# Performance work log

Hardware: AMD Instinct MI355X
Metric: run time of the kernel (lower is better)

Reference implementation:

```python
import jax, jax.numpy as jnp
import numpy as np

NB_CODE = 1024
N, CODE_DIM, T = 32, 512, 2048


def setup_inputs() -> dict:
    key = jax.random.key(0)
    k1, k2 = jax.random.split(key)
    x = jax.random.normal(k1, (N, CODE_DIM, T), dtype=jnp.float32)
    codebook = jax.random.normal(k2, (NB_CODE, CODE_DIM), dtype=jnp.float32)
    return {"x": x, "codebook": codebook}


def reference(x, codebook):
    n, c, t = x.shape
    # preprocess: 'n c t -> (n t) c'
    xf = jnp.transpose(x, (0, 2, 1)).reshape(n * t, c)  # (NT, C)
    dist = (
        jnp.sum(xf * xf, axis=-1, keepdims=True)
        - 2.0 * jnp.matmul(xf, codebook.T)
        + jnp.sum(codebook * codebook, axis=-1)[None, :]
    )
    # gumbel_sample(-distance) with training=False -> plain argmax(-dist) = argmin(dist)
    code_idx = jnp.argmin(dist, axis=-1)  # (NT,) int32
    # dequantize: embedding gather
    x_d = codebook[code_idx]  # (NT, C)
    # compute_perplexity (eval path)
    counts = jax.ops.segment_sum(
        jnp.ones_like(code_idx, dtype=jnp.float32), code_idx, num_segments=NB_CODE
    )
    prob = counts / jnp.sum(counts)
    perplexity = jnp.exp(-jnp.sum(prob * jnp.log(prob + 1e-7)))
    # commit loss against detached quantized codes
    commit_loss = jnp.mean(jnp.square(xf - jax.lax.stop_gradient(x_d)))
    # straight-through estimator
    x_st = xf + jax.lax.stop_gradient(x_d - xf)
    x_out = jnp.transpose(x_st.reshape(n, t, c), (0, 2, 1))  # (N, C, T)
    return x_out, commit_loss, perplexity
```

## Files before the change

### kernel.cpp

```cpp
#include <hip/hip_runtime.h>
#include <stdint.h>

#define N_  32
#define C_  512
#define T_  2048
#define NB  1024
#define NT  (N_ * T_)
#define GB_S 129

typedef _Float16 h8 __attribute__((ext_vector_type(8)));
typedef _Float16 h4 __attribute__((ext_vector_type(4)));
typedef float    f4 __attribute__((ext_vector_type(4)));

#define WS_COMMIT   0
#define WS_COUNTS   64
#define WS_CNORM    4224
#define WS_RMIN     8320
#define WS_CBH      532608
#define WS_CBL      1581184
#define WS_XTH      2629760
#define WS_XTL      69738624
#define WS_NEED     136847488ull

__device__ __forceinline__ void gll16(const void* g, void* l) {
    __builtin_amdgcn_global_load_lds((const __attribute__((address_space(1))) void*)g,
                                     (__attribute__((address_space(3))) void*)l, 16, 0, 0);
}

__global__ void k_initA(unsigned* ws32, unsigned long long* rmin) {
    int g = blockIdx.x * 256 + threadIdx.x;
    if (g < 1040) ws32[g] = 0u;
    rmin[g] = 0xFFFFFFFFFFFFFFFFull;
}

__global__ void k_initS(unsigned* ws32) {
    int g = blockIdx.x * 256 + threadIdx.x;
    if (g < 1040) ws32[g] = 0u;
}

__global__ void k_codenorm(const float* __restrict__ cb, float* __restrict__ cnorm) {
    int j = blockIdx.x * 256 + threadIdx.x;
    const float* r = cb + (size_t)j * C_;
    float s = 0.f;
    for (int i = 0; i < C_; i += 4) {
        float4 v = *(const float4*)&r[i];
        s = fmaf(v.x, v.x, s); s = fmaf(v.y, v.y, s);
        s = fmaf(v.z, v.z, s); s = fmaf(v.w, v.w, s);
    }
    cnorm[j] = s;
}

__global__ void k_cvt_cb(const float* __restrict__ cb,
                         _Float16* __restrict__ cbh, _Float16* __restrict__ cbl) {
    int t = blockIdx.x * 256 + threadIdx.x;
    float4 v = *(const float4*)&cb[(size_t)t * 4];
    h4 hi, lo;
    hi.x = (_Float16)v.x; lo.x = (_Float16)(v.x - (float)hi.x);
    hi.y = (_Float16)v.y; lo.y = (_Float16)(v.y - (float)hi.y);
    hi.z = (_Float16)v.z; lo.z = (_Float16)(v.z - (float)hi.z);
    hi.w = (_Float16)v.w; lo.w = (_Float16)(v.w - (float)hi.w);
    *(h4*)&cbh[(size_t)t * 4] = hi;
    *(h4*)&cbl[(size_t)t * 4] = lo;
}

__global__ __launch_bounds__(256)
void k_xt(const float* __restrict__ x,
          _Float16* __restrict__ xth, _Float16* __restrict__ xtl) {
    __shared__ float Ls[64 * 68];
    const int bx = blockIdx.x;
    const int n = bx >> 8;
    const int cblk = (bx >> 5) & 7, tblk = bx & 31;
    const int c0 = cblk * 64, t0 = tblk * 64;
    const int tid = threadIdx.x;
    #pragma unroll
    for (int ld = 0; ld < 4; ++ld) {
        int idx = tid + ld * 256;
        int cc = idx >> 4, t4 = (idx & 15) << 2;
        float4 v = *(const float4*)&x[((size_t)n * C_ + c0 + cc) * T_ + t0 + t4];
        *(float4*)&Ls[cc * 68 + t4] = v;
    }
    __syncthreads();
    const int tt = tid >> 2, cs = (tid & 3) * 16;
    h8 hi0, hi1, lo0, lo1;
    #pragma unroll
    for (int j = 0; j < 8; ++j) {
        float f = Ls[(cs + j) * 68 + tt];
        _Float16 h = (_Float16)f;
        hi0[j] = h; lo0[j] = (_Float16)(f - (float)h);
    }
    #pragma unroll
    for (int j = 0; j < 8; ++j) {
        float f = Ls[(cs + 8 + j) * 68 + tt];
        _Float16 h = (_Float16)f;
        hi1[j] = h; lo1[j] = (_Float16)(f - (float)h);
    }
    const size_t dst = ((size_t)n * T_ + t0 + tt) * C_ + c0 + cs;
    *(h8*)&xth[dst] = hi0; *(h8*)&xth[dst + 8] = hi1;
    *(h8*)&xtl[dst] = lo0; *(h8*)&xtl[dst + 8] = lo1;
}

__global__ __launch_bounds__(256, 2)
void k_gemm(const _Float16* __restrict__ xth, const _Float16* __restrict__ xtl,
            const _Float16* __restrict__ cbh, const _Float16* __restrict__ cbl,
            const float* __restrict__ cnorm, unsigned long long* __restrict__ rmin) {
    __shared__ _Float16 sm[24576];
    const int tid = threadIdx.x;
    const int l = tid & 63, w = tid >> 6;
    const int q = l >> 4, r = l & 15;
    const int wm0 = (w & 1) * 64, wn0 = (w >> 1) * 128;
    const int bid = blockIdx.x;
    const int lrow = l >> 2;
    const int lcolB = (l & 3) * 16;

    const char* gAh = (const char*)xth + ((size_t)bid * 128 + w * 16 + lrow) * 1024 + lcolB;
    const char* gAl = (const char*)xtl + ((size_t)bid * 128 + w * 16 + lrow) * 1024 + lcolB;

    const int aoff = (wm0 + r) * 32 + q * 8;
    const int boff = (wn0 + r) * 32 + q * 8;

    for (int ch = 0; ch < 4; ++ch) {
        const int j0 = ch * 256;
        const char* gBh = (const char*)cbh + ((size_t)j0 + w * 16 + lrow) * 1024 + lcolB;
        const char* gBl = (const char*)cbl + ((size_t)j0 + w * 16 + lrow) * 1024 + lcolB;

        f4 acc[4][8];
        #pragma unroll
        for (int i = 0; i < 4; ++i)
            #pragma unroll
            for (int j = 0; j < 8; ++j)
                acc[i][j] = (f4){0.f, 0.f, 0.f, 0.f};

        for (int kb = 0; kb < 16; ++kb) {
            const int kof = kb * 64;
            __syncthreads();
            gll16(gAh + kof,         &sm[(size_t)w * 512]);
            gll16(gAh + 65536 + kof, &sm[(size_t)(4 + w) * 512]);
            gll16(gAl + kof,         &sm[4096 + (size_t)w * 512]);
            gll16(gAl + 65536 + kof, &sm[4096 + (size_t)(4 + w) * 512]);
            #pragma unroll
            for (int p = 0; p < 4; ++p) {
                gll16(gBh + (size_t)p * 65536 + kof, &sm[8192  + (size_t)(p * 4 + w) * 512]);
                gll16(gBl + (size_t)p * 65536 + kof, &sm[16384 + (size_t)(p * 4 + w) * 512]);
            }
            __syncthreads();

            h8 ah[4], al[4];
            #pragma unroll
            for (int i = 0; i < 4; ++i) {
                ah[i] = *(const h8*)&sm[aoff + i * 512];
                al[i] = *(const h8*)&sm[4096 + aoff + i * 512];
            }
            #pragma unroll
            for (int j = 0; j < 8; ++j) {
                h8 bh = *(const h8*)&sm[8192  + boff + j * 512];
                h8 bl = *(const h8*)&sm[16384 + boff + j * 512];
                #pragma unroll
                for (int i = 0; i < 4; ++i) {
                    acc[i][j] = __builtin_amdgcn_mfma_f32_16x16x32_f16(ah[i], bh, acc[i][j], 0, 0, 0);
                    acc[i][j] = __builtin_amdgcn_mfma_f32_16x16x32_f16(al[i], bh, acc[i][j], 0, 0, 0);
                    acc[i][j] = __builtin_amdgcn_mfma_f32_16x16x32_f16(ah[i], bl, acc[i][j], 0, 0, 0);
                }
            }
        }

        float cn[8];
        #pragma unroll
        for (int j = 0; j < 8; ++j) cn[j] = cnorm[j0 + wn0 + j * 16 + r];

        #pragma unroll
        for (int i = 0; i < 4; ++i) {
            #pragma unroll
            for (int rg = 0; rg < 4; ++rg) {
                unsigned long long best = 0xFFFFFFFFFFFFFFFFull;
                #pragma unroll
                for (int j = 0; j < 8; ++j) {
                    float s = fmaf(-2.0f, acc[i][j][rg], cn[j]);
                    unsigned u = __float_as_uint(s);
                    u = (u & 0x80000000u) ? ~u : (u | 0x80000000u);
                    unsigned long long key =
                        ((unsigned long long)u << 32) | (unsigned)(j0 + wn0 + j * 16 + r);
                    best = key < best ? key : best;
                }
                #pragma unroll
                for (int off = 1; off < 16; off <<= 1) {
                    unsigned long long o = __shfl_xor(best, off, 64);
                    best = o < best ? o : best;
                }
                if (r == 0)
                    atomicMin(&rmin[(size_t)bid * 128 + wm0 + i * 16 + q * 4 + rg], best);
            }
        }
    }
}

__global__ __launch_bounds__(256)
void k_post(const float* __restrict__ x, const float* __restrict__ cb,
            const unsigned long long* __restrict__ rmin,
            float* __restrict__ out, float* __restrict__ commitAcc,
            int* __restrict__ counts) {
    __shared__ float gbuf[64 * GB_S];
    __shared__ int sidx[128];
    __shared__ float red[4];
    const int bid = blockIdx.x;
    const int tid = threadIdx.x;
    const size_t r0 = (size_t)bid * 128;
    const int n  = (int)(r0 >> 11);
    const int t0 = (int)(r0 & 2047);
    const size_t xbase = (size_t)n * C_ * T_ + t0;

    if (tid < 128) {
        int code = (int)(rmin[r0 + tid] & 0xFFFFFFFFull);
        sidx[tid] = code;
        atomicAdd(&counts[code], 1);
    }
    __syncthreads();

    const int tl   = tid >> 1;
    const int half = tid & 1;
    const int tcol  = tid & 127;
    const int chalf = tid >> 7;
    float commit = 0.f;

    for (int c0 = 0; c0 < C_; c0 += 64) {
        __syncthreads();
        const int code = sidx[tl];
        const float* src = &cb[(size_t)code * C_ + c0 + half * 32];
        #pragma unroll
        for (int qq = 0; qq < 8; ++qq) {
            float4 v = *(const float4*)&src[qq * 4];
            const int cc = half * 32 + qq * 4;
            gbuf[(cc + 0) * GB_S + tl] = v.x;
            gbuf[(cc + 1) * GB_S + tl] = v.y;
            gbuf[(cc + 2) * GB_S + tl] = v.z;
            gbuf[(cc + 3) * GB_S + tl] = v.w;
        }
        __syncthreads();
        #pragma unroll 8
        for (int i = 0; i < 32; ++i) {
            const int cc = i * 2 + chalf;
            const size_t gidx = xbase + (size_t)(c0 + cc) * T_ + tcol;
            float g  = gbuf[cc * GB_S + tcol];
            float xv = x[gidx];
            out[gidx] = g;
            float d = xv - g;
            commit = fmaf(d, d, commit);
        }
    }

    #pragma unroll
    for (int off = 32; off; off >>= 1) commit += __shfl_down(commit, off, 64);
    if ((tid & 63) == 0) red[tid >> 6] = commit;
    __syncthreads();
    if (tid == 0) atomicAdd(commitAcc, red[0] + red[1] + red[2] + red[3]);
}

__global__ void k_final(const int* __restrict__ counts,
                        const float* __restrict__ commitAcc,
                        float* __restrict__ out) {
    __shared__ float red[4];
    int tid = threadIdx.x;
    float s = 0.f;
    for (int j = tid; j < NB; j += 256) {
        float p = (float)counts[j] * (1.0f / (float)NT);
        s += p * logf(p + 1e-7f);
    }
    #pragma unroll
    for (int off = 32; off; off >>= 1) s += __shfl_down(s, off, 64);
    if ((tid & 63) == 0) red[tid >> 6] = s;
    __syncthreads();
    if (tid == 0) {
        float H = red[0] + red[1] + red[2] + red[3];
        out[(size_t)NT * C_]     = commitAcc[0] * (1.0f / ((float)NT * (float)C_));
        out[(size_t)NT * C_ + 1] = expf(-H);
    }
}

#define BM  128
#define BN  128
#define BK  16
#define AS_S 128
#define BS_S 132

__global__ __launch_bounds__(256, 4)
void k_main_fb(const float* __restrict__ x, const float* __restrict__ cb,
               const float* __restrict__ cnorm, float* __restrict__ out,
               float* __restrict__ commitAcc, int* __restrict__ counts) {
    __shared__ float smem[8256];
    __shared__ unsigned long long rmin[BM];
    __shared__ int sidx[BM];
    __shared__ float red[4];

    float* As = smem;
    float* Bs = smem + BK * AS_S;

    const int bid = blockIdx.x;
    const int n   = bid >> 4;
    const int t0  = (bid & 15) << 7;
    const int tid = threadIdx.x;
    const int tx  = tid & 15;
    const int ty  = tid >> 4;

    if (tid < BM) rmin[tid] = 0xFFFFFFFFFFFFFFFFull;

    const size_t xbase = (size_t)n * C_ * T_ + t0;

    for (int ch = 0; ch < NB / BN; ++ch) {
        const int j0 = ch * BN;
        float acc[2][2][4][4];
        #pragma unroll
        for (int a0 = 0; a0 < 2; ++a0)
            #pragma unroll
            for (int a1 = 0; a1 < 2; ++a1)
                #pragma unroll
                for (int a2 = 0; a2 < 4; ++a2)
                    #pragma unroll
                    for (int a3 = 0; a3 < 4; ++a3) acc[a0][a1][a2][a3] = 0.f;

        for (int kb = 0; kb < C_ / BK; ++kb) {
            const int k0 = kb * BK;
            __syncthreads();
            {
                const int kk = tid >> 5;
                const int m4 = (tid & 31) << 2;
                float4 a0v = *(const float4*)&x[xbase + (size_t)(k0 + kk) * T_ + m4];
                float4 a1v = *(const float4*)&x[xbase + (size_t)(k0 + kk + 8) * T_ + m4];
                *(float4*)&As[kk * AS_S + m4] = a0v;
                *(float4*)&As[(kk + 8) * AS_S + m4] = a1v;
                const int j  = tid >> 2;
                const int kq = (tid & 3) << 2;
                float4 b0v = *(const float4*)&cb[(size_t)(j0 + j) * C_ + k0 + kq];
                float4 b1v = *(const float4*)&cb[(size_t)(j0 + j + 64) * C_ + k0 + kq];
                Bs[(kq + 0) * BS_S + j] = b0v.x;
                Bs[(kq + 1) * BS_S + j] = b0v.y;
                Bs[(kq + 2) * BS_S + j] = b0v.z;
                Bs[(kq + 3) * BS_S + j] = b0v.w;
                Bs[(kq + 0) * BS_S + j + 64] = b1v.x;
                Bs[(kq + 1) * BS_S + j + 64] = b1v.y;
                Bs[(kq + 2) * BS_S + j + 64] = b1v.z;
                Bs[(kq + 3) * BS_S + j + 64] = b1v.w;
            }
            __syncthreads();
            #pragma unroll
            for (int kk = 0; kk < BK; ++kk) {
                float4 aL = *(const float4*)&As[kk * AS_S + (ty << 2)];
                float4 aH = *(const float4*)&As[kk * AS_S + 64 + (ty << 2)];
                float4 bL = *(const float4*)&Bs[kk * BS_S + (tx << 2)];
                float4 bH = *(const float4*)&Bs[kk * BS_S + 64 + (tx << 2)];
                float av[2][4] = {{aL.x, aL.y, aL.z, aL.w}, {aH.x, aH.y, aH.z, aH.w}};
                float bv[2][4] = {{bL.x, bL.y, bL.z, bL.w}, {bH.x, bH.y, bH.z, bH.w}};
                #pragma unroll
                for (int ih = 0; ih < 2; ++ih)
                    #pragma unroll
                    for (int i = 0; i < 4; ++i)
                        #pragma unroll
                        for (int jh = 0; jh < 2; ++jh)
                            #pragma unroll
                            for (int j = 0; j < 4; ++j)
                                acc[ih][jh][i][j] = fmaf(av[ih][i], bv[jh][j], acc[ih][jh][i][j]);
            }
        }

        float cnj[2][4];
        #pragma unroll
        for (int jh = 0; jh < 2; ++jh)
            #pragma unroll
            for (int j = 0; j < 4; ++j)
                cnj[jh][j] = cnorm[j0 + jh * 64 + (tx << 2) + j];

        #pragma unroll
        for (int ih = 0; ih < 2; ++ih) {
            #pragma unroll
            for (int i = 0; i < 4; ++i) {
                const int row = ih * 64 + (ty << 2) + i;
                unsigned long long best = 0xFFFFFFFFFFFFFFFFull;
                #pragma unroll
                for (int jh = 0; jh < 2; ++jh) {
                    #pragma unroll
                    for (int j = 0; j < 4; ++j) {
                        const int code = j0 + jh * 64 + (tx << 2) + j;
                        float s = fmaf(-2.0f, acc[ih][jh][i][j], cnj[jh][j]);
                        unsigned u = __float_as_uint(s);
                        u = (u & 0x80000000u) ? ~u : (u | 0x80000000u);
                        unsigned long long key =
                            ((unsigned long long)u << 32) | (unsigned)code;
                        best = key < best ? key : best;
                    }
                }
                #pragma unroll
                for (int off = 8; off; off >>= 1) {
                    unsigned long long o = __shfl_down(best, off, 16);
                    best = o < best ? o : best;
                }
                if (tx == 0) {
                    unsigned long long cur = rmin[row];
                    rmin[row] = best < cur ? best : cur;
                }
            }
        }
    }

    __syncthreads();
    if (tid < BM) {
        int code = (int)(rmin[tid] & 0xFFFFFFFFull);
        sidx[tid] = code;
        atomicAdd(&counts[code], 1);
    }
    __syncthreads();

    float* gbuf = smem;
    const int tl   = tid >> 1;
    const int half = tid & 1;
    const int tcol  = tid & 127;
    const int chalf = tid >> 7;
    float commit = 0.f;

    for (int c0 = 0; c0 < C_; c0 += 64) {
        __syncthreads();
        const int code = sidx[tl];
        const float* src = &cb[(size_t)code * C_ + c0 + half * 32];
        #pragma unroll
        for (int qq = 0; qq < 8; ++qq) {
            float4 v = *(const float4*)&src[qq * 4];
            const int cc = half * 32 + qq * 4;
            gbuf[(cc + 0) * GB_S + tl] = v.x;
            gbuf[(cc + 1) * GB_S + tl] = v.y;
            gbuf[(cc + 2) * GB_S + tl] = v.z;
            gbuf[(cc + 3) * GB_S + tl] = v.w;
        }
        __syncthreads();
        #pragma unroll 8
        for (int i = 0; i < 32; ++i) {
            const int cc = i * 2 + chalf;
            const size_t gidx = xbase + (size_t)(c0 + cc) * T_ + tcol;
            float g  = gbuf[cc * GB_S + tcol];
            float xv = x[gidx];
            out[gidx] = g;
            float d = xv - g;
            commit = fmaf(d, d, commit);
        }
    }

    #pragma unroll
    for (int off = 32; off; off >>= 1) commit += __shfl_down(commit, off, 64);
    if ((tid & 63) == 0) red[tid >> 6] = commit;
    __syncthreads();
    if (tid == 0) atomicAdd(commitAcc, red[0] + red[1] + red[2] + red[3]);
}

extern "C" void kernel_launch(void* const* d_in, const int* in_sizes, int n_in,
                              void* d_out, int out_size, void* d_ws, size_t ws_size,
                              hipStream_t stream) {
    const float* x  = (const float*)d_in[0];
    const float* cb = (const float*)d_in[1];
    float* out = (float*)d_out;

    char* ws = (char*)d_ws;
    float* commitAcc = (float*)(ws + WS_COMMIT);
    int*   counts    = (int*)(ws + WS_COUNTS);
    float* cnorm     = (float*)(ws + WS_CNORM);
    unsigned long long* rmin = (unsigned long long*)(ws + WS_RMIN);
    _Float16* cbh = (_Float16*)(ws + WS_CBH);
    _Float16* cbl = (_Float16*)(ws + WS_CBL);
    _Float16* xth = (_Float16*)(ws + WS_XTH);
    _Float16* xtl = (_Float16*)(ws + WS_XTL);

    if (ws_size >= WS_NEED) {
        k_initA<<<256, 256, 0, stream>>>((unsigned*)ws, rmin);
        k_codenorm<<<4, 256, 0, stream>>>(cb, cnorm);
        k_cvt_cb<<<512, 256, 0, stream>>>(cb, cbh, cbl);
        k_xt<<<8192, 256, 0, stream>>>(x, xth, xtl);
        k_gemm<<<512, 256, 0, stream>>>(xth, xtl, cbh, cbl, cnorm, rmin);
        k_post<<<512, 256, 0, stream>>>(x, cb, rmin, out, commitAcc, counts);
        k_final<<<1, 256, 0, stream>>>(counts, commitAcc, out);
    } else {
        k_initS<<<5, 256, 0, stream>>>((unsigned*)ws);
        k_codenorm<<<4, 256, 0, stream>>>(cb, cnorm);
        k_main_fb<<<512, 256, 0, stream>>>(x, cb, cnorm, out, commitAcc, counts);
        k_final<<<1, 256, 0, stream>>>(counts, commitAcc, out);
    }
}
```

Measured before the change: 544.7 us.

## Retile split-fp16 GEMM with double-buffered LDS and derive commit loss from distances

```diff
diff --git a/kernel.cpp b/kernel.cpp
--- a/kernel.cpp
+++ b/kernel.cpp
@@ -13,6 +13,7 @@
 typedef float    f4 __attribute__((ext_vector_type(4)));
 
 #define WS_COMMIT   0
+#define WS_SUMSQ    8
 #define WS_COUNTS   64
 #define WS_CNORM    4224
 #define WS_RMIN     8320
@@ -65,8 +66,10 @@
 
 __global__ __launch_bounds__(256)
 void k_xt(const float* __restrict__ x,
-          _Float16* __restrict__ xth, _Float16* __restrict__ xtl) {
+          _Float16* __restrict__ xth, _Float16* __restrict__ xtl,
+          float* __restrict__ sumsq) {
     __shared__ float Ls[64 * 68];
+    __shared__ float sred[4];
     const int bx = blockIdx.x;
     const int n = bx >> 8;
     const int cblk = (bx >> 5) & 7, tblk = bx & 31;
@@ -82,119 +85,143 @@
     __syncthreads();
     const int tt = tid >> 2, cs = (tid & 3) * 16;
     h8 hi0, hi1, lo0, lo1;
+    float ss = 0.f;
     #pragma unroll
     for (int j = 0; j < 8; ++j) {
         float f = Ls[(cs + j) * 68 + tt];
+        ss = fmaf(f, f, ss);
         _Float16 h = (_Float16)f;
         hi0[j] = h; lo0[j] = (_Float16)(f - (float)h);
     }
     #pragma unroll
     for (int j = 0; j < 8; ++j) {
         float f = Ls[(cs + 8 + j) * 68 + tt];
+        ss = fmaf(f, f, ss);
         _Float16 h = (_Float16)f;
         hi1[j] = h; lo1[j] = (_Float16)(f - (float)h);
     }
     const size_t dst = ((size_t)n * T_ + t0 + tt) * C_ + c0 + cs;
     *(h8*)&xth[dst] = hi0; *(h8*)&xth[dst + 8] = hi1;
     *(h8*)&xtl[dst] = lo0; *(h8*)&xtl[dst + 8] = lo1;
-}
-
-__global__ __launch_bounds__(256, 2)
+    #pragma unroll
+    for (int off = 32; off; off >>= 1) ss += __shfl_down(ss, off, 64);
+    if ((tid & 63) == 0) sred[tid >> 6] = ss;
+    __syncthreads();
+    if (tid == 0) atomicAdd(sumsq, sred[0] + sred[1] + sred[2] + sred[3]);
+}
+
+__global__ __launch_bounds__(512, 2)
 void k_gemm(const _Float16* __restrict__ xth, const _Float16* __restrict__ xtl,
             const _Float16* __restrict__ cbh, const _Float16* __restrict__ cbl,
             const float* __restrict__ cnorm, unsigned long long* __restrict__ rmin) {
-    __shared__ _Float16 sm[24576];
+    __shared__ __attribute__((aligned(128))) char smc[131072];
     const int tid = threadIdx.x;
     const int l = tid & 63, w = tid >> 6;
     const int q = l >> 4, r = l & 15;
-    const int wm0 = (w & 1) * 64, wn0 = (w >> 1) * 128;
+
     const int bid = blockIdx.x;
-    const int lrow = l >> 2;
-    const int lcolB = (l & 3) * 16;
-
-    const char* gAh = (const char*)xth + ((size_t)bid * 128 + w * 16 + lrow) * 1024 + lcolB;
-    const char* gAl = (const char*)xtl + ((size_t)bid * 128 + w * 16 + lrow) * 1024 + lcolB;
-
-    const int aoff = (wm0 + r) * 32 + q * 8;
-    const int boff = (wn0 + r) * 32 + q * 8;
-
-    for (int ch = 0; ch < 4; ++ch) {
-        const int j0 = ch * 256;
-        const char* gBh = (const char*)cbh + ((size_t)j0 + w * 16 + lrow) * 1024 + lcolB;
-        const char* gBl = (const char*)cbl + ((size_t)j0 + w * 16 + lrow) * 1024 + lcolB;
-
-        f4 acc[4][8];
-        #pragma unroll
-        for (int i = 0; i < 4; ++i)
-            #pragma unroll
-            for (int j = 0; j < 8; ++j)
-                acc[i][j] = (f4){0.f, 0.f, 0.f, 0.f};
-
-        for (int kb = 0; kb < 16; ++kb) {
-            const int kof = kb * 64;
-            __syncthreads();
-            gll16(gAh + kof,         &sm[(size_t)w * 512]);
-            gll16(gAh + 65536 + kof, &sm[(size_t)(4 + w) * 512]);
-            gll16(gAl + kof,         &sm[4096 + (size_t)w * 512]);
-            gll16(gAl + 65536 + kof, &sm[4096 + (size_t)(4 + w) * 512]);
-            #pragma unroll
-            for (int p = 0; p < 4; ++p) {
-                gll16(gBh + (size_t)p * 65536 + kof, &sm[8192  + (size_t)(p * 4 + w) * 512]);
-                gll16(gBl + (size_t)p * 65536 + kof, &sm[16384 + (size_t)(p * 4 + w) * 512]);
+    const int swz = (bid & 7) * 128 + (bid >> 3);
+    const int mb = swz >> 2, nb = swz & 3;
+
+    const char* xthc = (const char*)xth;
+    const char* xtlc = (const char*)xtl;
+    const char* cbhc = (const char*)cbh;
+    const char* cblc = (const char*)cbl;
+
+    const int g16 = l >> 2;
+    const int sslot = ((l & 3) ^ (g16 & 3)) << 4;
+    const int s = w >> 1;
+    const int rhalf = (w & 1) * 128;
+    const char* sbase = (s == 0) ? xthc : (s == 1) ? xtlc : (s == 2) ? cbhc : cblc;
+    const int rowblk = (s < 2) ? (mb * 256) : (nb * 256);
+    const size_t srcOff = ((size_t)(rowblk + rhalf + g16)) * 1024 + sslot;
+    const int ldsOff = s * 16384 + rhalf * 64;
+
+    const int wmi = w & 3, wni = w >> 2;
+    const int slq = (q ^ (r & 3)) << 4;
+    const int aoffb = (wmi * 64 + r) * 64 + slq;
+    const int boffb = 32768 + (wni * 128 + r) * 64 + slq;
+
+    f4 acc[4][8];
+    #pragma unroll
+    for (int i = 0; i < 4; ++i)
+        #pragma unroll
+        for (int j = 0; j < 8; ++j) acc[i][j] = (f4){0.f, 0.f, 0.f, 0.f};
+
+#define STAGE_T(tt, bb) { \
+    const char* sp_ = sbase + srcOff + (tt) * 64; \
+    char* dp_ = smc + (bb) + ldsOff; \
+    _Pragma("unroll") \
+    for (int c_ = 0; c_ < 8; ++c_) gll16(sp_ + c_ * 16384, dp_ + c_ * 1024); }
+
+    STAGE_T(0, 0);
+    asm volatile("s_waitcnt vmcnt(0)" ::: "memory");
+    __builtin_amdgcn_s_barrier();
+
+    int b0 = 0;
+    #pragma unroll 2
+    for (int t = 0; t < 16; ++t) {
+        if (t < 15) STAGE_T(t + 1, b0 ^ 65536);
+        h8 ah[4], al[4];
+        #pragma unroll
+        for (int mf = 0; mf < 4; ++mf) {
+            ah[mf] = *(const h8*)(smc + b0 + aoffb + mf * 1024);
+            al[mf] = *(const h8*)(smc + b0 + 16384 + aoffb + mf * 1024);
+        }
+        __builtin_amdgcn_s_setprio(1);
+        #pragma unroll
+        for (int nf = 0; nf < 8; ++nf) {
+            h8 bhf = *(const h8*)(smc + b0 + boffb + nf * 1024);
+            h8 blf = *(const h8*)(smc + b0 + 16384 + boffb + nf * 1024);
+            #pragma unroll
+            for (int mf = 0; mf < 4; ++mf) {
+                acc[mf][nf] = __builtin_amdgcn_mfma_f32_16x16x32_f16(ah[mf], bhf, acc[mf][nf], 0, 0, 0);
+                acc[mf][nf] = __builtin_amdgcn_mfma_f32_16x16x32_f16(al[mf], bhf, acc[mf][nf], 0, 0, 0);
+                acc[mf][nf] = __builtin_amdgcn_mfma_f32_16x16x32_f16(ah[mf], blf, acc[mf][nf], 0, 0, 0);
             }
-            __syncthreads();
-
-            h8 ah[4], al[4];
-            #pragma unroll
-            for (int i = 0; i < 4; ++i) {
-                ah[i] = *(const h8*)&sm[aoff + i * 512];
-                al[i] = *(const h8*)&sm[4096 + aoff + i * 512];
+        }
+        __builtin_amdgcn_s_setprio(0);
+        if (t < 15) {
+            asm volatile("s_waitcnt vmcnt(0)" ::: "memory");
+            __builtin_amdgcn_s_barrier();
+            b0 ^= 65536;
+        }
+    }
+#undef STAGE_T
+
+    const int codeBase = nb * 256 + wni * 128;
+    const int rowBase  = mb * 256 + wmi * 64;
+    float cn[8];
+    #pragma unroll
+    for (int nf = 0; nf < 8; ++nf) cn[nf] = cnorm[codeBase + nf * 16 + r];
+
+    #pragma unroll
+    for (int mf = 0; mf < 4; ++mf) {
+        #pragma unroll
+        for (int rg = 0; rg < 4; ++rg) {
+            unsigned long long best = 0xFFFFFFFFFFFFFFFFull;
+            #pragma unroll
+            for (int nf = 0; nf < 8; ++nf) {
+                float sc = fmaf(-2.0f, acc[mf][nf][rg], cn[nf]);
+                unsigned u = __float_as_uint(sc);
+                u = (u & 0x80000000u) ? ~u : (u | 0x80000000u);
+                unsigned long long key =
+                    ((unsigned long long)u << 32) | (unsigned)(codeBase + nf * 16 + r);
+                best = key < best ? key : best;
             }
             #pragma unroll
-            for (int j = 0; j < 8; ++j) {
-                h8 bh = *(const h8*)&sm[8192  + boff + j * 512];
-                h8 bl = *(const h8*)&sm[16384 + boff + j * 512];
-                #pragma unroll
-                for (int i = 0; i < 4; ++i) {
-                    acc[i][j] = __builtin_amdgcn_mfma_f32_16x16x32_f16(ah[i], bh, acc[i][j], 0, 0, 0);
-                    acc[i][j] = __builtin_amdgcn_mfma_f32_16x16x32_f16(al[i], bh, acc[i][j], 0, 0, 0);
-                    acc[i][j] = __builtin_amdgcn_mfma_f32_16x16x32_f16(ah[i], bl, acc[i][j], 0, 0, 0);
-                }
+            for (int off = 1; off < 16; off <<= 1) {
+                unsigned long long o = __shfl_xor(best, off, 64);
+                best = o < best ? o : best;
             }
-        }
-
-        float cn[8];
-        #pragma unroll
-        for (int j = 0; j < 8; ++j) cn[j] = cnorm[j0 + wn0 + j * 16 + r];
-
-        #pragma unroll
-        for (int i = 0; i < 4; ++i) {
-            #pragma unroll
-            for (int rg = 0; rg < 4; ++rg) {
-                unsigned long long best = 0xFFFFFFFFFFFFFFFFull;
-                #pragma unroll
-                for (int j = 0; j < 8; ++j) {
-                    float s = fmaf(-2.0f, acc[i][j][rg], cn[j]);
-                    unsigned u = __float_as_uint(s);
-                    u = (u & 0x80000000u) ? ~u : (u | 0x80000000u);
-                    unsigned long long key =
-                        ((unsigned long long)u << 32) | (unsigned)(j0 + wn0 + j * 16 + r);
-                    best = key < best ? key : best;
-                }
-                #pragma unroll
-                for (int off = 1; off < 16; off <<= 1) {
-                    unsigned long long o = __shfl_xor(best, off, 64);
-                    best = o < best ? o : best;
-                }
-                if (r == 0)
-                    atomicMin(&rmin[(size_t)bid * 128 + wm0 + i * 16 + q * 4 + rg], best);
-            }
+            if (r == 0)
+                atomicMin(&rmin[rowBase + mf * 16 + q * 4 + rg], best);
         }
     }
 }
 
 __global__ __launch_bounds__(256)
-void k_post(const float* __restrict__ x, const float* __restrict__ cb,
+void k_post(const float* __restrict__ cb,
             const unsigned long long* __restrict__ rmin,
             float* __restrict__ out, float* __restrict__ commitAcc,
             int* __restrict__ counts) {
@@ -208,18 +235,26 @@
     const int t0 = (int)(r0 & 2047);
     const size_t xbase = (size_t)n * C_ * T_ + t0;
 
+    float sc = 0.f;
     if (tid < 128) {
-        int code = (int)(rmin[r0 + tid] & 0xFFFFFFFFull);
+        unsigned long long key = rmin[r0 + tid];
+        int code = (int)(key & 0xFFFFFFFFull);
         sidx[tid] = code;
         atomicAdd(&counts[code], 1);
-    }
-    __syncthreads();
+        unsigned up = (unsigned)(key >> 32);
+        unsigned ub = (up & 0x80000000u) ? (up & 0x7FFFFFFFu) : ~up;
+        sc = __uint_as_float(ub);
+    }
+    #pragma unroll
+    for (int off = 32; off; off >>= 1) sc += __shfl_down(sc, off, 64);
+    if ((tid & 63) == 0) red[tid >> 6] = sc;
+    __syncthreads();
+    if (tid == 0) atomicAdd(commitAcc, red[0] + red[1] + red[2] + red[3]);
 
     const int tl   = tid >> 1;
     const int half = tid & 1;
     const int tcol  = tid & 127;
     const int chalf = tid >> 7;
-    float commit = 0.f;
 
     for (int c0 = 0; c0 < C_; c0 += 64) {
         __syncthreads();
@@ -239,23 +274,14 @@
         for (int i = 0; i < 32; ++i) {
             const int cc = i * 2 + chalf;
             const size_t gidx = xbase + (size_t)(c0 + cc) * T_ + tcol;
-            float g  = gbuf[cc * GB_S + tcol];
-            float xv = x[gidx];
-            out[gidx] = g;
-            float d = xv - g;
-            commit = fmaf(d, d, commit);
-        }
-    }
-
-    #pragma unroll
-    for (int off = 32; off; off >>= 1) commit += __shfl_down(commit, off, 64);
-    if ((tid & 63) == 0) red[tid >> 6] = commit;
-    __syncthreads();
-    if (tid == 0) atomicAdd(commitAcc, red[0] + red[1] + red[2] + red[3]);
+            out[gidx] = gbuf[cc * GB_S + tcol];
+        }
+    }
 }
 
 __global__ void k_final(const int* __restrict__ counts,
                         const float* __restrict__ commitAcc,
+                        const float* __restrict__ sumsq,
                         float* __restrict__ out) {
     __shared__ float red[4];
     int tid = threadIdx.x;
@@ -270,7 +296,7 @@
     __syncthreads();
     if (tid == 0) {
         float H = red[0] + red[1] + red[2] + red[3];
-        out[(size_t)NT * C_]     = commitAcc[0] * (1.0f / ((float)NT * (float)C_));
+        out[(size_t)NT * C_]     = (commitAcc[0] + sumsq[0]) * (1.0f / ((float)NT * (float)C_));
         out[(size_t)NT * C_ + 1] = expf(-H);
     }
 }
@@ -456,6 +482,7 @@
 
     char* ws = (char*)d_ws;
     float* commitAcc = (float*)(ws + WS_COMMIT);
+    float* sumsq     = (float*)(ws + WS_SUMSQ);
     int*   counts    = (int*)(ws + WS_COUNTS);
     float* cnorm     = (float*)(ws + WS_CNORM);
     unsigned long long* rmin = (unsigned long long*)(ws + WS_RMIN);
@@ -468,14 +495,14 @@
         k_initA<<<256, 256, 0, stream>>>((unsigned*)ws, rmin);
         k_codenorm<<<4, 256, 0, stream>>>(cb, cnorm);
         k_cvt_cb<<<512, 256, 0, stream>>>(cb, cbh, cbl);
-        k_xt<<<8192, 256, 0, stream>>>(x, xth, xtl);
-        k_gemm<<<512, 256, 0, stream>>>(xth, xtl, cbh, cbl, cnorm, rmin);
-        k_post<<<512, 256, 0, stream>>>(x, cb, rmin, out, commitAcc, counts);
-        k_final<<<1, 256, 0, stream>>>(counts, commitAcc, out);
+        k_xt<<<8192, 256, 0, stream>>>(x, xth, xtl, sumsq);
+        k_gemm<<<1024, 512, 0, stream>>>(xth, xtl, cbh, cbl, cnorm, rmin);
+        k_post<<<512, 256, 0, stream>>>(cb, rmin, out, commitAcc, counts);
+        k_final<<<1, 256, 0, stream>>>(counts, commitAcc, sumsq, out);
     } else {
         k_initS<<<5, 256, 0, stream>>>((unsigned*)ws);
         k_codenorm<<<4, 256, 0, stream>>>(cb, cnorm);
         k_main_fb<<<512, 256, 0, stream>>>(x, cb, cnorm, out, commitAcc, counts);
-        k_final<<<1, 256, 0, stream>>>(counts, commitAcc, out);
-    }
-}
+        k_final<<<1, 256, 0, stream>>>(counts, commitAcc, sumsq, out);
+    }
+}
```

Measured after the change: 540.1 us. No clear change (-0.8%).
